# Kernel tuning notes

Measured on AMD Instinct MI355X. Metric: run time of the kernel, lower is better.

The kernel has to match this reference:

```python
import jax, jax.numpy as jnp
import numpy as np

N_LAYERS = 2
NUM_SAMPLES = 64
GAIN = 1.0
RENDER_DIM = 16


def _sample_plane(plane, u, v):
    # plane: [C,H,W]; u,v: [R,S] coords in [-1,1] (clamped / border padding)
    # returns bilinear features [R,S,C] (align_corners=True grid_sample semantics)
    C, H, W = plane.shape
    x = (jnp.clip(u, -1.0, 1.0) + 1.0) * 0.5 * (W - 1)
    y = (jnp.clip(v, -1.0, 1.0) + 1.0) * 0.5 * (H - 1)
    x0 = jnp.clip(jnp.floor(x).astype(jnp.int32), 0, W - 2)
    y0 = jnp.clip(jnp.floor(y).astype(jnp.int32), 0, H - 2)
    wx = (x - x0)[None]  # [1,R,S]
    wy = (y - y0)[None]
    f = (plane[:, y0, x0] * (1 - wx) * (1 - wy)
         + plane[:, y0, x0 + 1] * wx * (1 - wy)
         + plane[:, y0 + 1, x0] * (1 - wx) * wy
         + plane[:, y0 + 1, x0 + 1] * wx * wy)  # [C,R,S]
    return jnp.moveaxis(f, 0, -1)


def _sample_triplane(pxy, pyz, pzx, pts):
    x, y, z = pts[..., 0], pts[..., 1], pts[..., 2]
    return (_sample_plane(pxy, x, y) + _sample_plane(pyz, y, z)
            + _sample_plane(pzx, z, x))


def _forward(xy, yz, zx, xy_color, yz_color, zx_color, mlp_weights, mlp_biases,
             weight_opacity, bias_opacity, weight_color, bias_color,
             rays, centers, rays_encoding, near, far, bg_color):
    S = NUM_SAMPLES
    step = (jnp.arange(S, dtype=rays.dtype) + 0.5) / S
    t = near[..., None] + (far - near)[..., None] * step        # [B,R,S]
    delta = ((far - near) / S)[..., None]                        # [B,R,1]
    pts = centers[:, :, None, :] + t[..., None] * rays[:, :, None, :]  # [B,R,S,3]
    sample = jax.vmap(_sample_triplane)
    h = sample(xy, yz, zx, pts)                                  # [B,R,S,C]
    for l in range(N_LAYERS):
        h = jax.nn.softplus(GAIN * (h @ mlp_weights[l] + mlp_biases[l]))
    sigma = jax.nn.softplus(GAIN * (h @ weight_opacity + bias_opacity[0]))  # [B,R,S]
    fc = sample(xy_color, yz_color, zx_color, pts)
    color = (h + fc + rays_encoding[:, :, None, :]) @ weight_color + bias_color
    sd = sigma * delta                                           # sigma_i * delta_i
    csd = jnp.cumsum(sd, axis=-1)
    nlt = csd[..., -1]                                           # -log transmittance
    w = jnp.exp(sd - csd) * (1.0 - jnp.exp(-sd))                 # T_i * alpha_i
    feat = jnp.einsum('brs,brsk->brk', w, color)
    ray_len = jnp.sum(w * t, axis=-1)
    mask = 1.0 - jnp.exp(-nlt)
    feat = feat[..., :RENDER_DIM] + (1.0 - mask)[..., None] * bg_color
    return feat, mask, ray_len


def setup_inputs() -> dict:
    key = jax.random.key(0)
    ks = jax.random.split(key, 16)
    B, R, C, HW, KRD = 2, 8192, 64, 256, 16
    plane = lambda k: jax.random.normal(k, (B, C, HW, HW), jnp.float32) * 0.5
    d = jax.random.normal(ks[0], (B, R, 3), jnp.float32)
    rays = d / jnp.linalg.norm(d, axis=-1, keepdims=True)
    centers = jax.random.uniform(ks[1], (B, R, 3), jnp.float32, -0.3, 0.3)
    near = jax.random.uniform(ks[2], (B, R), jnp.float32, 0.1, 0.5)
    far = near + jax.random.uniform(ks[3], (B, R), jnp.float32, 1.5, 2.5)
    xavier = lambda k, shp: jax.random.normal(k, shp, jnp.float32) * np.float32(np.sqrt(2.0 / (shp[-2] + shp[-1])))
    return {
        'rays': rays, 'centers': centers,
        'rays_encoding': jax.random.normal(ks[4], (B, R, C), jnp.float32) * 0.1,
        'near': near, 'far': far,
        'xy': plane(ks[5]), 'yz': plane(ks[6]), 'zx': plane(ks[7]),
        'xy_color': plane(ks[8]), 'yz_color': plane(ks[9]), 'zx_color': plane(ks[10]),
        'mlp_weights': xavier(ks[11], (N_LAYERS, C, C)),
        'mlp_biases': jnp.zeros((N_LAYERS, C), jnp.float32),
        'weight_opacity': jax.random.uniform(ks[12], (C,), jnp.float32, -1.0 / np.sqrt(C), 1.0 / np.sqrt(C)),
        'bias_opacity': jnp.full((1,), -1.0, jnp.float32),
        'weight_color': xavier(ks[13], (C, KRD)),
        'bias_color': jnp.zeros((KRD,), jnp.float32),
        'bg_color': jnp.zeros((RENDER_DIM,), jnp.float32),
    }


def reference(rays, centers, rays_encoding, near, far, xy, yz, zx,
              xy_color, yz_color, zx_color, mlp_weights, mlp_biases,
              weight_opacity, bias_opacity, weight_color, bias_color, bg_color):
    return _forward(xy, yz, zx, xy_color, yz_color, zx_color, mlp_weights,
                    mlp_biases, weight_opacity, bias_opacity, weight_color,
                    bias_color, rays, centers, rays_encoding, near, far, bg_color)
```

## Files before the change

### kernel.cpp

```cpp
#include <hip/hip_runtime.h>
#include <hip/hip_bf16.h>

typedef unsigned short ushort_t;
typedef unsigned int   uint_t;
typedef __attribute__((ext_vector_type(8))) _Float16 half8;
typedef __attribute__((ext_vector_type(2))) _Float16 half2v;
typedef __attribute__((ext_vector_type(4))) float    floatx4;

#define B_    2
#define R_    8192
#define HW_   256
#define S_    64
#define NRAYS (B_*R_)
#define PLANE_ELEMS ((size_t)64*HW_*HW_)
#define NTEX  ((size_t)HW_*HW_)
#define WS_PLANES_BYTES (6ull*B_*NTEX*64*2)
#define NW_US 10240
#define WV 4
#define NWG (NRAYS/WV)
#define NBINS 1024

#define WS_WQ_OFF   WS_PLANES_BYTES
#define WS_KEYS_OFF (WS_WQ_OFF + NW_US*2)
#define WS_PERM_OFF (WS_KEYS_OFF + NRAYS*4)
#define WS_HIST_OFF (WS_PERM_OFF + NRAYS*4)
#define WS_OFFS_OFF (WS_HIST_OFF + NBINS*4)

__device__ __forceinline__ float sp(float x){ return fmaxf(x, 0.f) + __logf(1.f + __expf(-fabsf(x))); }
__device__ __forceinline__ ushort_t f2h(float f){
    union{_Float16 h; ushort_t u;} v; v.h = (_Float16)f; return v.u;
}
__device__ __forceinline__ half2v splat_h2(float w){
    return __builtin_bit_cast(half2v, __builtin_amdgcn_cvt_pkrtz(w, w));
}

__global__ __launch_bounds__(256) void tr_planes(
    const float* __restrict__ p0, const float* __restrict__ p1, const float* __restrict__ p2,
    const float* __restrict__ p3, const float* __restrict__ p4, const float* __restrict__ p5,
    ushort_t* __restrict__ outp)
{
    __shared__ ushort_t st[128*136];
    const int blk = blockIdx.x;
    const int xh = blk & 1, y = (blk >> 1) & 255, b = (blk >> 9) & 1, pidx = blk >> 10;
    const int tid = threadIdx.x;
    const int xt = tid >> 1;
    const int half = tid & 1;
    const int p = pidx + half*3;
    const float* src = (p==0)?p0:(p==1)?p1:(p==2)?p2:(p==3)?p3:(p==4)?p4:p5;
    src += (size_t)b*PLANE_ELEMS + (size_t)y*HW_ + (size_t)(xh*128 + xt);

    ushort_t* row = &st[xt*136 + half*64];
#pragma unroll
    for (int c = 0; c < 64; ++c)
        row[c] = f2h(src[(size_t)c*HW_*HW_]);
    __syncthreads();

    ushort_t* dst = outp + ((size_t)(pidx*2+b)*NTEX + (size_t)y*HW_ + (size_t)xh*128)*128;
#pragma unroll
    for (int i = 0; i < 8; ++i) {
        const int idx = i*256 + tid;
        const int rec = idx >> 4;
        const int within = (idx & 15)*16;
        uint4 v = *reinterpret_cast<const uint4*>(
            reinterpret_cast<const char*>(st) + rec*272 + within);
        reinterpret_cast<uint4*>(dst)[idx] = v;
    }
}

__global__ __launch_bounds__(256) void prep_weights(
    const float* __restrict__ mlp_w, const float* __restrict__ w_op,
    const float* __restrict__ w_col, ushort_t* __restrict__ dst)
{
    int i = blockIdx.x*256 + threadIdx.x;
    if (i >= NW_US) return;
    float v;
    if (i < 8192) {
        int l = i >> 12, o = (i >> 6) & 63, c = i & 63;
        v = mlp_w[l*4096 + c*64 + o];
    } else {
        int j = i - 8192, n = j >> 6, c = j & 63;
        v = (n < 16) ? w_col[c*16 + n] : (n == 16 ? w_op[c] : 0.f);
    }
    dst[i] = f2h(v);
}

__global__ __launch_bounds__(256) void ray_keys(
    const float* __restrict__ rays, const float* __restrict__ centers,
    const float* __restrict__ nearp, const float* __restrict__ farp,
    uint_t* __restrict__ keys, uint_t* __restrict__ hist)
{
    int rid = blockIdx.x*256 + threadIdx.x;
    if (rid >= NRAYS) return;
    const float t = 0.5f*(nearp[rid] + farp[rid]);
    float c[3];
#pragma unroll
    for (int a = 0; a < 3; ++a) {
        float p = centers[rid*3+a] + t*rays[rid*3+a];
        p = fminf(fmaxf(p, -1.f), 1.f);
        int ci = (int)((p + 1.f)*4.f);
        c[a] = (float)(ci > 7 ? 7 : ci);
    }
    uint_t key = (uint_t)(rid >> 13)*512 + (uint_t)c[2]*64 + (uint_t)c[1]*8 + (uint_t)c[0];
    keys[rid] = key;
    atomicAdd(&hist[key], 1u);
}

__global__ __launch_bounds__(NBINS) void scan_hist(
    const uint_t* __restrict__ hist, uint_t* __restrict__ offs)
{
    __shared__ uint_t tmp[NBINS];
    const int tid = threadIdx.x;
    const uint_t own = hist[tid];
    tmp[tid] = own;
    __syncthreads();
#pragma unroll
    for (int off = 1; off < NBINS; off <<= 1) {
        uint_t v = (tid >= off) ? tmp[tid - off] : 0u;
        __syncthreads();
        tmp[tid] += v;
        __syncthreads();
    }
    offs[tid] = tmp[tid] - own;
}

__global__ __launch_bounds__(256) void scatter_perm(
    const uint_t* __restrict__ keys, uint_t* __restrict__ offs, uint_t* __restrict__ perm)
{
    int rid = blockIdx.x*256 + threadIdx.x;
    if (rid >= NRAYS) return;
    uint_t pos = atomicAdd(&offs[keys[rid]], 1u);
    perm[pos] = (uint_t)rid;
}

__global__ __launch_bounds__(256) void render(
    const float* __restrict__ rays, const float* __restrict__ centers,
    const float* __restrict__ enc,  const float* __restrict__ nearp, const float* __restrict__ farp,
    const float* __restrict__ mlp_b, const float* __restrict__ b_op,
    const float* __restrict__ b_col, const float* __restrict__ bgc,
    const ushort_t* __restrict__ trp, const ushort_t* __restrict__ wq,
    const uint_t* __restrict__ perm, float* __restrict__ out)
{
    __shared__ ushort_t A_lds[WV][4096];
    __shared__ float    sd_lds[WV][64];
    __shared__ float    w_lds [WV][64];

    const int wv = threadIdx.x >> 6, lane = threadIdx.x & 63;
    const int sg = lane >> 3, ch = lane & 7;
    const int sb  = (blockIdx.x & 7)*(NWG/8) + (blockIdx.x >> 3);
    const int rid = (int)perm[sb*WV + wv];
    const int b = rid >> 13;
    ushort_t* A = &A_lds[wv][0];

    const float nr = nearp[rid], fr = farp[rid];
    const float rdx = rays[rid*3+0], rdy = rays[rid*3+1], rdz = rays[rid*3+2];
    const float rox = centers[rid*3+0], roy = centers[rid*3+1], roz = centers[rid*3+2];
    const float delta = (fr - nr) * (1.f/S_);
    const float t  = nr + (fr - nr) * ((lane + 0.5f) * (1.f/S_));

    auto ldfrag = [&](int mi, int kt) -> half8 {
        int m  = mi*16 + (lane&15);
        int cb = (kt*64 + ((lane>>4)*16)) ^ ((m&7)<<4);
        return *reinterpret_cast<const half8*>(reinterpret_cast<const char*>(A) + m*128 + cb);
    };
    auto ldbfrag = [&](const ushort_t* wrow, int nt, int kt) -> half8 {
        return *reinterpret_cast<const half8*>(wrow + (nt*16 + (lane&15))*64 + kt*32 + (lane>>4)*8);
    };
    auto stH = [&](int m, int n, float v) {
        A[(m*128 + ((n*2) ^ ((m&7)<<4))) >> 1] = f2h(v);
    };

    auto mlp_layer = [&](const ushort_t* wrow, const float* bias) {
        half8 af[8];
#pragma unroll
        for (int mi = 0; mi < 4; ++mi)
#pragma unroll
            for (int kt = 0; kt < 2; ++kt) af[mi*2+kt] = ldfrag(mi, kt);
#pragma unroll
        for (int nt = 0; nt < 4; ++nt) {
            half8 b0 = ldbfrag(wrow, nt, 0);
            half8 b1 = ldbfrag(wrow, nt, 1);
            floatx4 acc[4];
#pragma unroll
            for (int mi = 0; mi < 4; ++mi) {
                acc[mi] = (floatx4){0.f,0.f,0.f,0.f};
                acc[mi] = __builtin_amdgcn_mfma_f32_16x16x32_f16(af[mi*2+0], b0, acc[mi], 0, 0, 0);
                acc[mi] = __builtin_amdgcn_mfma_f32_16x16x32_f16(af[mi*2+1], b1, acc[mi], 0, 0, 0);
            }
            const int n = nt*16 + (lane&15);
            const float bc = bias[n];
#pragma unroll
            for (int mi = 0; mi < 4; ++mi)
#pragma unroll
                for (int r = 0; r < 4; ++r) {
                    int m = mi*16 + (lane>>4)*4 + r;
                    stH(m, n, sp(acc[mi][r] + bc));
                }
        }
    };

    const ushort_t* whead = wq + 8192;

    half2v accD[8][4];
#pragma unroll
    for (int j = 0; j < 8; ++j)
#pragma unroll
        for (int k = 0; k < 4; ++k) accD[j][k] = half2v{(_Float16)0.f, (_Float16)0.f};
    half2v i0, i1, i2, i3;
    {
        const float* er = enc + (size_t)rid*64 + ch*8;
        float4 e0 = *reinterpret_cast<const float4*>(er);
        float4 e1 = *reinterpret_cast<const float4*>(er + 4);
        i0 = half2v{(_Float16)e0.x, (_Float16)e0.y};
        i1 = half2v{(_Float16)e0.z, (_Float16)e0.w};
        i2 = half2v{(_Float16)e1.x, (_Float16)e1.y};
        i3 = half2v{(_Float16)e1.z, (_Float16)e1.w};
    }
#pragma unroll
    for (int j = 0; j < 8; ++j) {
        half2v accC[4] = {i0, i1, i2, i3};
        const int s = j*8 + sg;
        const float ts = nr + (fr - nr) * ((s + 0.5f) * (1.f/S_));
        const float qx = rox + ts*rdx, qy = roy + ts*rdy, qz = roz + ts*rdz;
        const float uu[3] = {qx, qy, qz};
        const float vv[3] = {qy, qz, qx};
#pragma unroll
        for (int p = 0; p < 3; ++p) {
            float x = (fminf(fmaxf(uu[p],-1.f),1.f) + 1.f) * 127.5f;
            float y = (fminf(fmaxf(vv[p],-1.f),1.f) + 1.f) * 127.5f;
            int x0 = (int)floorf(x); x0 = x0 < 0 ? 0 : (x0 > 254 ? 254 : x0);
            int y0 = (int)floorf(y); y0 = y0 < 0 ? 0 : (y0 > 254 ? 254 : y0);
            const int pp = y0*HW_ + x0;
            const float fx = x - (float)x0, fy = y - (float)y0;
            const half2v w00 = splat_h2((1.f-fx)*(1.f-fy));
            const half2v w01 = splat_h2(fx*(1.f-fy));
            const half2v w10 = splat_h2((1.f-fx)*fy);
            const half2v w11 = splat_h2(fx*fy);
            const ushort_t* lb = trp + ((size_t)(p*2+b)*NTEX + (size_t)pp)*128 + ch*8;
            union { uint4 v; half2v h[4]; } d00,d01,d10,d11, c00,c01,c10,c11;
            d00.v = *reinterpret_cast<const uint4*>(lb);
            c00.v = *reinterpret_cast<const uint4*>(lb + 64);
            d01.v = *reinterpret_cast<const uint4*>(lb + 128);
            c01.v = *reinterpret_cast<const uint4*>(lb + 192);
            d10.v = *reinterpret_cast<const uint4*>(lb + 128*HW_);
            c10.v = *reinterpret_cast<const uint4*>(lb + 128*HW_ + 64);
            d11.v = *reinterpret_cast<const uint4*>(lb + 128*HW_ + 128);
            c11.v = *reinterpret_cast<const uint4*>(lb + 128*HW_ + 192);
#pragma unroll
            for (int k = 0; k < 4; ++k) {
                accD[j][k] += w00*d00.h[k] + w01*d01.h[k] + w10*d10.h[k] + w11*d11.h[k];
                accC[k]    += w00*c00.h[k] + w01*c01.h[k] + w10*c10.h[k] + w11*c11.h[k];
            }
        }
        union { half2v h[4]; uint4 v; } pk;
#pragma unroll
        for (int k = 0; k < 4; ++k) pk.h[k] = accC[k];
        *reinterpret_cast<uint4*>(reinterpret_cast<char*>(A) + s*128 + ((ch*16) ^ (sg<<4))) = pk.v;
    }

    floatx4 accH[4];
#pragma unroll
    for (int mi = 0; mi < 4; ++mi) accH[mi] = (floatx4){0.f,0.f,0.f,0.f};
    {
        half8 b0 = ldbfrag(whead, 0, 0);
        half8 b1 = ldbfrag(whead, 0, 1);
#pragma unroll
        for (int mi = 0; mi < 4; ++mi) {
            accH[mi] = __builtin_amdgcn_mfma_f32_16x16x32_f16(ldfrag(mi,0), b0, accH[mi], 0, 0, 0);
            accH[mi] = __builtin_amdgcn_mfma_f32_16x16x32_f16(ldfrag(mi,1), b1, accH[mi], 0, 0, 0);
        }
    }

#pragma unroll
    for (int j = 0; j < 8; ++j) {
        union { half2v h[4]; uint4 v; } pk;
#pragma unroll
        for (int k = 0; k < 4; ++k) pk.h[k] = accD[j][k];
        const int s = j*8 + sg;
        *reinterpret_cast<uint4*>(reinterpret_cast<char*>(A) + s*128 + ((ch*16) ^ (sg<<4))) = pk.v;
    }

    mlp_layer(wq,        mlp_b);
    mlp_layer(wq + 4096, mlp_b + 64);

    half8 af[8];
#pragma unroll
    for (int mi = 0; mi < 4; ++mi)
#pragma unroll
        for (int kt = 0; kt < 2; ++kt) af[mi*2+kt] = ldfrag(mi, kt);

    {
        half8 b0 = ldbfrag(whead, 1, 0);
        half8 b1 = ldbfrag(whead, 1, 1);
        floatx4 accS[4];
#pragma unroll
        for (int mi = 0; mi < 4; ++mi) {
            accS[mi] = (floatx4){0.f,0.f,0.f,0.f};
            accS[mi] = __builtin_amdgcn_mfma_f32_16x16x32_f16(af[mi*2+0], b0, accS[mi], 0, 0, 0);
            accS[mi] = __builtin_amdgcn_mfma_f32_16x16x32_f16(af[mi*2+1], b1, accS[mi], 0, 0, 0);
        }
        if ((lane & 15) == 0) {
            const float bop = b_op[0];
#pragma unroll
            for (int mi = 0; mi < 4; ++mi)
#pragma unroll
                for (int r = 0; r < 4; ++r) {
                    int m = mi*16 + (lane>>4)*4 + r;
                    sd_lds[wv][m] = sp(accS[mi][r] + bop) * delta;
                }
        }
    }

    {
        half8 b0 = ldbfrag(whead, 0, 0);
        half8 b1 = ldbfrag(whead, 0, 1);
#pragma unroll
        for (int mi = 0; mi < 4; ++mi) {
            accH[mi] = __builtin_amdgcn_mfma_f32_16x16x32_f16(af[mi*2+0], b0, accH[mi], 0, 0, 0);
            accH[mi] = __builtin_amdgcn_mfma_f32_16x16x32_f16(af[mi*2+1], b1, accH[mi], 0, 0, 0);
        }
    }

    const float sdv = sd_lds[wv][lane];
    float csd = sdv;
#pragma unroll
    for (int off = 1; off < 64; off <<= 1) {
        float nn = __shfl_up(csd, off, 64);
        if (lane >= off) csd += nn;
    }
    const float nlt = __shfl(csd, 63, 64);
    const float Tw  = __expf(sdv - csd) * (1.f - __expf(-sdv));
    const float em  = __expf(-nlt);
    w_lds[wv][lane] = Tw;

    float rl = Tw * t;
#pragma unroll
    for (int off = 32; off > 0; off >>= 1) rl += __shfl_xor(rl, off, 64);

    const float bcn = b_col[lane & 15];
    float pf = 0.f;
#pragma unroll
    for (int mi = 0; mi < 4; ++mi)
#pragma unroll
        for (int r = 0; r < 4; ++r) {
            int m = mi*16 + (lane>>4)*4 + r;
            pf += w_lds[wv][m] * (accH[mi][r] + bcn);
        }
    pf += __shfl_xor(pf, 16, 64);
    pf += __shfl_xor(pf, 32, 64);

    if (lane < 16)
        out[(size_t)rid*16 + lane] = pf + em * bgc[lane];
    if (lane == 0) {
        out[(size_t)NRAYS*16 + rid] = 1.f - em;
        out[(size_t)NRAYS*17 + rid] = rl;
    }
}

extern "C" void kernel_launch(void* const* d_in, const int* in_sizes, int n_in,
                              void* d_out, int out_size, void* d_ws, size_t ws_size,
                              hipStream_t stream)
{
    const float* rays    = (const float*)d_in[0];
    const float* centers = (const float*)d_in[1];
    const float* enc     = (const float*)d_in[2];
    const float* nearp   = (const float*)d_in[3];
    const float* farp    = (const float*)d_in[4];
    const float* xy      = (const float*)d_in[5];
    const float* yz      = (const float*)d_in[6];
    const float* zx      = (const float*)d_in[7];
    const float* xyc     = (const float*)d_in[8];
    const float* yzc     = (const float*)d_in[9];
    const float* zxc     = (const float*)d_in[10];
    const float* mlp_w   = (const float*)d_in[11];
    const float* mlp_b   = (const float*)d_in[12];
    const float* w_op    = (const float*)d_in[13];
    const float* b_op    = (const float*)d_in[14];
    const float* w_col   = (const float*)d_in[15];
    const float* b_col   = (const float*)d_in[16];
    const float* bg      = (const float*)d_in[17];
    float* out = (float*)d_out;

    char* ws = (char*)d_ws;
    ushort_t* trp  = (ushort_t*)ws;
    ushort_t* wq   = (ushort_t*)(ws + WS_WQ_OFF);
    uint_t*   keys = (uint_t*)(ws + WS_KEYS_OFF);
    uint_t*   perm = (uint_t*)(ws + WS_PERM_OFF);
    uint_t*   hist = (uint_t*)(ws + WS_HIST_OFF);
    uint_t*   offs = (uint_t*)(ws + WS_OFFS_OFF);

    tr_planes<<<3*2*HW_*2, 256, 0, stream>>>(xy, yz, zx, xyc, yzc, zxc, trp);
    prep_weights<<<(NW_US + 255)/256, 256, 0, stream>>>(mlp_w, w_op, w_col, wq);

    hipMemsetAsync(hist, 0, NBINS*sizeof(uint_t), stream);
    ray_keys<<<NRAYS/256, 256, 0, stream>>>(rays, centers, nearp, farp, keys, hist);
    scan_hist<<<1, NBINS, 0, stream>>>(hist, offs);
    scatter_perm<<<NRAYS/256, 256, 0, stream>>>(keys, offs, perm);

    render<<<NWG, WV*64, 0, stream>>>(
        rays, centers, enc, nearp, farp, mlp_b, b_op, b_col, bg, trp, wq, perm, out);
}
```

Before: 270.4 us.

## Transpose MFMA operands in render MLP and halve waves per block

Swaps the MFMA operand roles so weights are the A operand and per-sample activations the B operand. Each lane's accumulator then holds four consecutive output channels for one sample, which lets the softplus results be packed and written to LDS as 8-byte stores instead of scattered 2-byte stores. The color reduction now uses shuffles instead of an LDS weight buffer and writes float4 outputs. The color bias is folded out as bias times opacity. Blocks shrink from 4 to 2 waves, which changes occupancy and scheduling granularity.

```diff
diff --git a/kernel.cpp b/kernel.cpp
--- a/kernel.cpp
+++ b/kernel.cpp
@@ -16,7 +16,7 @@
 #define NTEX  ((size_t)HW_*HW_)
 #define WS_PLANES_BYTES (6ull*B_*NTEX*64*2)
 #define NW_US 10240
-#define WV 4
+#define WV 2
 #define NWG (NRAYS/WV)
 #define NBINS 1024
 
@@ -132,7 +132,7 @@
     perm[pos] = (uint_t)rid;
 }
 
-__global__ __launch_bounds__(256) void render(
+__global__ __launch_bounds__(WV*64) void render(
     const float* __restrict__ rays, const float* __restrict__ centers,
     const float* __restrict__ enc,  const float* __restrict__ nearp, const float* __restrict__ farp,
     const float* __restrict__ mlp_b, const float* __restrict__ b_op,
@@ -142,7 +142,6 @@
 {
     __shared__ ushort_t A_lds[WV][4096];
     __shared__ float    sd_lds[WV][64];
-    __shared__ float    w_lds [WV][64];
 
     const int wv = threadIdx.x >> 6, lane = threadIdx.x & 63;
     const int sg = lane >> 3, ch = lane & 7;
@@ -157,44 +156,40 @@
     const float delta = (fr - nr) * (1.f/S_);
     const float t  = nr + (fr - nr) * ((lane + 0.5f) * (1.f/S_));
 
-    auto ldfrag = [&](int mi, int kt) -> half8 {
-        int m  = mi*16 + (lane&15);
-        int cb = (kt*64 + ((lane>>4)*16)) ^ ((m&7)<<4);
-        return *reinterpret_cast<const half8*>(reinterpret_cast<const char*>(A) + m*128 + cb);
+    auto ldfrag = [&](int stile, int kt) -> half8 {
+        int s  = stile*16 + (lane&15);
+        int cb = (kt*64 + ((lane>>4)*16)) ^ ((s&7)<<4);
+        return *reinterpret_cast<const half8*>(reinterpret_cast<const char*>(A) + s*128 + cb);
     };
-    auto ldbfrag = [&](const ushort_t* wrow, int nt, int kt) -> half8 {
+    auto ldwfrag = [&](const ushort_t* wrow, int nt, int kt) -> half8 {
         return *reinterpret_cast<const half8*>(wrow + (nt*16 + (lane&15))*64 + kt*32 + (lane>>4)*8);
     };
-    auto stH = [&](int m, int n, float v) {
-        A[(m*128 + ((n*2) ^ ((m&7)<<4))) >> 1] = f2h(v);
-    };
-
-    auto mlp_layer = [&](const ushort_t* wrow, const float* bias) {
-        half8 af[8];
-#pragma unroll
-        for (int mi = 0; mi < 4; ++mi)
-#pragma unroll
-            for (int kt = 0; kt < 2; ++kt) af[mi*2+kt] = ldfrag(mi, kt);
-#pragma unroll
-        for (int nt = 0; nt < 4; ++nt) {
-            half8 b0 = ldbfrag(wrow, nt, 0);
-            half8 b1 = ldbfrag(wrow, nt, 1);
-            floatx4 acc[4];
-#pragma unroll
-            for (int mi = 0; mi < 4; ++mi) {
-                acc[mi] = (floatx4){0.f,0.f,0.f,0.f};
-                acc[mi] = __builtin_amdgcn_mfma_f32_16x16x32_f16(af[mi*2+0], b0, acc[mi], 0, 0, 0);
-                acc[mi] = __builtin_amdgcn_mfma_f32_16x16x32_f16(af[mi*2+1], b1, acc[mi], 0, 0, 0);
+
+    auto mlp_layerT = [&](const ushort_t* wrow, const float* bias) {
+        half8 bf[8];
+#pragma unroll
+        for (int stile = 0; stile < 4; ++stile)
+#pragma unroll
+            for (int kt = 0; kt < 2; ++kt) bf[stile*2+kt] = ldfrag(stile, kt);
+#pragma unroll
+        for (int otile = 0; otile < 4; ++otile) {
+            half8 a0 = ldwfrag(wrow, otile, 0);
+            half8 a1 = ldwfrag(wrow, otile, 1);
+            float4 bb = *reinterpret_cast<const float4*>(bias + otile*16 + (lane>>4)*4);
+#pragma unroll
+            for (int stile = 0; stile < 4; ++stile) {
+                floatx4 acc = (floatx4){0.f,0.f,0.f,0.f};
+                acc = __builtin_amdgcn_mfma_f32_16x16x32_f16(a0, bf[stile*2+0], acc, 0, 0, 0);
+                acc = __builtin_amdgcn_mfma_f32_16x16x32_f16(a1, bf[stile*2+1], acc, 0, 0, 0);
+                const uint_t lo = __builtin_bit_cast(uint_t,
+                    __builtin_amdgcn_cvt_pkrtz(sp(acc[0]+bb.x), sp(acc[1]+bb.y)));
+                const uint_t hi = __builtin_bit_cast(uint_t,
+                    __builtin_amdgcn_cvt_pkrtz(sp(acc[2]+bb.z), sp(acc[3]+bb.w)));
+                const int s = stile*16 + (lane&15);
+                const int off = (otile*32 + ((lane>>4)*8)) ^ ((s&7)<<4);
+                *reinterpret_cast<uint2*>(reinterpret_cast<char*>(A) + s*128 + off)
+                    = make_uint2(lo, hi);
             }
-            const int n = nt*16 + (lane&15);
-            const float bc = bias[n];
-#pragma unroll
-            for (int mi = 0; mi < 4; ++mi)
-#pragma unroll
-                for (int r = 0; r < 4; ++r) {
-                    int m = mi*16 + (lane>>4)*4 + r;
-                    stH(m, n, sp(acc[mi][r] + bc));
-                }
         }
     };
 
@@ -258,15 +253,15 @@
     }
 
     floatx4 accH[4];
-#pragma unroll
-    for (int mi = 0; mi < 4; ++mi) accH[mi] = (floatx4){0.f,0.f,0.f,0.f};
     {
-        half8 b0 = ldbfrag(whead, 0, 0);
-        half8 b1 = ldbfrag(whead, 0, 1);
-#pragma unroll
-        for (int mi = 0; mi < 4; ++mi) {
-            accH[mi] = __builtin_amdgcn_mfma_f32_16x16x32_f16(ldfrag(mi,0), b0, accH[mi], 0, 0, 0);
-            accH[mi] = __builtin_amdgcn_mfma_f32_16x16x32_f16(ldfrag(mi,1), b1, accH[mi], 0, 0, 0);
+        half8 c0 = ldwfrag(whead, 0, 0);
+        half8 c1 = ldwfrag(whead, 0, 1);
+#pragma unroll
+        for (int stile = 0; stile < 4; ++stile) {
+            floatx4 acc = (floatx4){0.f,0.f,0.f,0.f};
+            acc = __builtin_amdgcn_mfma_f32_16x16x32_f16(c0, ldfrag(stile,0), acc, 0, 0, 0);
+            acc = __builtin_amdgcn_mfma_f32_16x16x32_f16(c1, ldfrag(stile,1), acc, 0, 0, 0);
+            accH[stile] = acc;
         }
     }
 
@@ -279,44 +274,36 @@
         *reinterpret_cast<uint4*>(reinterpret_cast<char*>(A) + s*128 + ((ch*16) ^ (sg<<4))) = pk.v;
     }
 
-    mlp_layer(wq,        mlp_b);
-    mlp_layer(wq + 4096, mlp_b + 64);
+    mlp_layerT(wq,        mlp_b);
+    mlp_layerT(wq + 4096, mlp_b + 64);
 
     half8 af[8];
 #pragma unroll
-    for (int mi = 0; mi < 4; ++mi)
-#pragma unroll
-        for (int kt = 0; kt < 2; ++kt) af[mi*2+kt] = ldfrag(mi, kt);
+    for (int stile = 0; stile < 4; ++stile)
+#pragma unroll
+        for (int kt = 0; kt < 2; ++kt) af[stile*2+kt] = ldfrag(stile, kt);
 
     {
-        half8 b0 = ldbfrag(whead, 1, 0);
-        half8 b1 = ldbfrag(whead, 1, 1);
-        floatx4 accS[4];
-#pragma unroll
-        for (int mi = 0; mi < 4; ++mi) {
-            accS[mi] = (floatx4){0.f,0.f,0.f,0.f};
-            accS[mi] = __builtin_amdgcn_mfma_f32_16x16x32_f16(af[mi*2+0], b0, accS[mi], 0, 0, 0);
-            accS[mi] = __builtin_amdgcn_mfma_f32_16x16x32_f16(af[mi*2+1], b1, accS[mi], 0, 0, 0);
-        }
-        if ((lane & 15) == 0) {
-            const float bop = b_op[0];
-#pragma unroll
-            for (int mi = 0; mi < 4; ++mi)
-#pragma unroll
-                for (int r = 0; r < 4; ++r) {
-                    int m = mi*16 + (lane>>4)*4 + r;
-                    sd_lds[wv][m] = sp(accS[mi][r] + bop) * delta;
-                }
+        half8 a0 = ldwfrag(whead, 1, 0);
+        half8 a1 = ldwfrag(whead, 1, 1);
+        const float bop = b_op[0];
+#pragma unroll
+        for (int stile = 0; stile < 4; ++stile) {
+            floatx4 acc = (floatx4){0.f,0.f,0.f,0.f};
+            acc = __builtin_amdgcn_mfma_f32_16x16x32_f16(a0, af[stile*2+0], acc, 0, 0, 0);
+            acc = __builtin_amdgcn_mfma_f32_16x16x32_f16(a1, af[stile*2+1], acc, 0, 0, 0);
+            if (lane < 16)
+                sd_lds[wv][stile*16 + lane] = sp(acc[0] + bop) * delta;
         }
     }
 
     {
-        half8 b0 = ldbfrag(whead, 0, 0);
-        half8 b1 = ldbfrag(whead, 0, 1);
-#pragma unroll
-        for (int mi = 0; mi < 4; ++mi) {
-            accH[mi] = __builtin_amdgcn_mfma_f32_16x16x32_f16(af[mi*2+0], b0, accH[mi], 0, 0, 0);
-            accH[mi] = __builtin_amdgcn_mfma_f32_16x16x32_f16(af[mi*2+1], b1, accH[mi], 0, 0, 0);
+        half8 c0 = ldwfrag(whead, 0, 0);
+        half8 c1 = ldwfrag(whead, 0, 1);
+#pragma unroll
+        for (int stile = 0; stile < 4; ++stile) {
+            accH[stile] = __builtin_amdgcn_mfma_f32_16x16x32_f16(c0, af[stile*2+0], accH[stile], 0, 0, 0);
+            accH[stile] = __builtin_amdgcn_mfma_f32_16x16x32_f16(c1, af[stile*2+1], accH[stile], 0, 0, 0);
         }
     }
 
@@ -330,28 +317,37 @@
     const float nlt = __shfl(csd, 63, 64);
     const float Tw  = __expf(sdv - csd) * (1.f - __expf(-sdv));
     const float em  = __expf(-nlt);
-    w_lds[wv][lane] = Tw;
+    const float mask = 1.f - em;
 
     float rl = Tw * t;
 #pragma unroll
     for (int off = 32; off > 0; off >>= 1) rl += __shfl_xor(rl, off, 64);
 
-    const float bcn = b_col[lane & 15];
-    float pf = 0.f;
-#pragma unroll
-    for (int mi = 0; mi < 4; ++mi)
-#pragma unroll
-        for (int r = 0; r < 4; ++r) {
-            int m = mi*16 + (lane>>4)*4 + r;
-            pf += w_lds[wv][m] * (accH[mi][r] + bcn);
-        }
-    pf += __shfl_xor(pf, 16, 64);
-    pf += __shfl_xor(pf, 32, 64);
-
-    if (lane < 16)
-        out[(size_t)rid*16 + lane] = pf + em * bgc[lane];
+    float pf[4] = {0.f, 0.f, 0.f, 0.f};
+#pragma unroll
+    for (int stile = 0; stile < 4; ++stile) {
+        const float wS = __shfl(Tw, stile*16 + (lane & 15), 64);
+#pragma unroll
+        for (int r = 0; r < 4; ++r) pf[r] += wS * accH[stile][r];
+    }
+#pragma unroll
+    for (int m = 1; m <= 8; m <<= 1)
+#pragma unroll
+        for (int r = 0; r < 4; ++r) pf[r] += __shfl_xor(pf[r], m, 64);
+
+    if ((lane & 15) == 0) {
+        const int o0 = (lane >> 4)*4;
+        float4 bc = *reinterpret_cast<const float4*>(b_col + o0);
+        float4 bg = *reinterpret_cast<const float4*>(bgc + o0);
+        float4 r;
+        r.x = pf[0] + bc.x*mask + em*bg.x;
+        r.y = pf[1] + bc.y*mask + em*bg.y;
+        r.z = pf[2] + bc.z*mask + em*bg.z;
+        r.w = pf[3] + bc.w*mask + em*bg.w;
+        *reinterpret_cast<float4*>(out + (size_t)rid*16 + o0) = r;
+    }
     if (lane == 0) {
-        out[(size_t)NRAYS*16 + rid] = 1.f - em;
+        out[(size_t)NRAYS*16 + rid] = mask;
         out[(size_t)NRAYS*17 + rid] = rl;
     }
 }
```

Result: faster. 258.1 us (-4.6%).
